# Performance work log

Hardware: AMD Instinct MI355X
Metric: run time of the kernel (lower is better)

## Reference

```python
import jax, jax.numpy as jnp
import numpy as np

N_ATOMS = 200000
N_EDGES = 6400000
N_TYPES = 4
COULOMB = 14.399645478425668  # e^2 / (4 pi eps0) in eV*Angstrom
P_EXP = 0.23
A0 = 0.4685


def _phi(r, c, da):
    # r: (E,), c: (4,), da: (4, E) -> (E,)
    return jnp.sum(c[:, None] * jnp.exp(-r * da), axis=0)


def _dphi(r, c, da):
    return jnp.sum(-c[:, None] * da * jnp.exp(-r * da), axis=0)


def _d2phi(r, c, da):
    return jnp.sum(c[:, None] * da ** 2 * jnp.exp(-r * da), axis=0)


def setup_inputs() -> dict:
    key = jax.random.key(0)
    k1, k2, k3, k4 = jax.random.split(key, 4)
    rij = jax.random.uniform(k1, (N_EDGES,), dtype=jnp.float32) * 2.0 + 0.1
    first_atom = jax.random.randint(k2, (N_EDGES,), 0, N_ATOMS, dtype=jnp.int32)
    second_atom = jax.random.randint(k3, (N_EDGES,), 0, N_ATOMS, dtype=jnp.int32)
    atom_type_index = jax.random.randint(k4, (N_ATOMS,), 0, N_TYPES, dtype=jnp.int32)
    # ASE covalent radii for H, C, N, O (Angstrom) and atomic numbers
    covalent_radii = jnp.array([0.31, 0.76, 0.71, 0.66], dtype=jnp.float32)
    atomic_numbers = jnp.array([1.0, 6.0, 7.0, 8.0], dtype=jnp.float32)
    return {
        "rij": rij,
        "covalent_radii": covalent_radii,
        "atomic_numbers": atomic_numbers,
        "first_atom": first_atom,
        "second_atom": second_atom,
        "atom_type_index": atom_type_index,
        "n_atoms": N_ATOMS,
    }


def reference(rij, covalent_radii, atomic_numbers, first_atom, second_atom, atom_type_index, n_atoms):
    # ZBL 4-term exponential screening coefficients
    c = jnp.array([0.02817, 0.28022, 0.50986, 0.18175], dtype=rij.dtype)
    d = jnp.array([0.20162, 0.4029, 0.94229, 3.1998], dtype=rij.dtype)

    ti = atom_type_index[first_atom]   # (E,)
    tj = atom_type_index[second_atom]  # (E,)
    zi = atomic_numbers[ti]
    zj = atomic_numbers[tj]
    rc = covalent_radii[ti] + covalent_radii[tj]  # outer cutoff per pair

    a = A0 / (zi ** P_EXP + zj ** P_EXP)  # (E,)
    da = d[:, None] / a                    # (4, E)
    factor = COULOMB * zi * zj             # (E,)

    # energy at rij
    e = factor / rij * _phi(rij, c, da)

    # switching polynomial matched at rc (r1 = 0)
    phi_c = _phi(rc, c, da)
    dphi_c = _dphi(rc, c, da)
    d2phi_c = _d2phi(rc, c, da)
    ec = factor / rc * phi_c
    dec = factor / rc * (-phi_c / rc + dphi_c)
    d2ec = factor / rc * (d2phi_c - 2.0 / rc * dphi_c + 2.0 * phi_c / rc ** 2)

    A = (-3.0 * dec + rc * d2ec) / rc ** 2
    B = (2.0 * dec - rc * d2ec) / rc ** 3
    C = -ec + rc * dec / 2.0 - rc * rc * d2ec / 12.0

    e = e + A / 3.0 * rij ** 3 + B / 4.0 * rij ** 4 + C
    e = e / 2.0
    e = jnp.where(rij > rc, jnp.zeros_like(e), e)

    # scatter pair energies onto first atom of each pair
    e_nodes = jax.ops.segment_sum(e, first_atom, num_segments=n_atoms)
    return e_nodes
```

## Files before the change

kernel.cpp:

```cpp
#include <hip/hip_runtime.h>

#define TPB_PACK  256
#define P1_BLOCKS 512
#define P1_TPB    512
#define SB_BITS   14
#define SBS       (1 << SB_BITS)
#define NS_MAX    16
#define P2_TPB    1024
#define R_SUB     24
#define TPB_RED   256
#define CAP_MAX   1024

__global__ __launch_bounds__(TPB_PACK) void zbl_pack(
    const int* __restrict__ types, unsigned int* __restrict__ packed,
    float* __restrict__ fallback, int natoms, int nwords)
{
    int tid = blockIdx.x * TPB_PACK + threadIdx.x;
    int nth = gridDim.x * TPB_PACK;
    for (int w = tid; w < nwords; w += nth) {
        int base = w << 4;
        unsigned int word = 0;
        #pragma unroll
        for (int j = 0; j < 16; ++j) {
            int i = base + j;
            unsigned int t = (i < natoms) ? (unsigned int)types[i] : 0u;
            word |= (t & 3u) << (2 * j);
        }
        packed[w] = word;
    }
    for (int i = tid; i < natoms; i += nth) fallback[i] = 0.0f;
}

__global__ __launch_bounds__(P1_TPB) void zbl_bin(
    const float* __restrict__ rij,
    const float* __restrict__ rcov,
    const float* __restrict__ znum,
    const int*  __restrict__ fa,
    const int*  __restrict__ sa,
    const unsigned int* __restrict__ packed,
    int2*  __restrict__ regions,
    int*   __restrict__ counts,
    float* __restrict__ fallback,
    int E, int nquad, int natoms, int nwords, int NS, int cap, int chunkQ)
{
    extern __shared__ unsigned int s_packed[];
    __shared__ float tab[9][16];
    __shared__ int scnt[NS_MAX];

    for (int w = threadIdx.x; w < nwords; w += P1_TPB)
        s_packed[w] = packed[w];
    if (threadIdx.x < NS) scnt[threadIdx.x] = 0;

    if (threadIdx.x < 16) {
        const float cc[4] = {0.02817f, 0.28022f, 0.50986f, 0.18175f};
        const float dd[4] = {0.20162f, 0.4029f, 0.94229f, 3.1998f};
        const float COUL = 14.399645478425668f;
        int t = threadIdx.x;
        int ti = t >> 2, tj = t & 3;
        float zi = znum[ti], zj = znum[tj];
        float rc = rcov[ti] + rcov[tj];
        float a = 0.4685f / (powf(zi, 0.23f) + powf(zj, 0.23f));
        float inva = 1.0f / a;
        float factor = COUL * zi * zj;
        float da[4], ee[4];
        float phi = 0.0f, dphi = 0.0f, d2phi = 0.0f;
        #pragma unroll
        for (int k = 0; k < 4; ++k) {
            da[k] = dd[k] * inva;
            ee[k] = expf(-rc * da[k]);
            phi   += cc[k] * ee[k];
            dphi  -= cc[k] * da[k] * ee[k];
            d2phi += cc[k] * da[k] * da[k] * ee[k];
        }
        float invrc = 1.0f / rc;
        float ec   = factor * invrc * phi;
        float dec  = factor * invrc * (-phi * invrc + dphi);
        float d2ec = factor * invrc * (d2phi - 2.0f * invrc * dphi + 2.0f * phi * invrc * invrc);
        float A = (-3.0f * dec + rc * d2ec) * invrc * invrc;
        float B = (2.0f * dec - rc * d2ec) * invrc * invrc * invrc;
        float Cc = -ec + 0.5f * rc * dec - rc * rc * d2ec * (1.0f / 12.0f);
        const float L2E = 1.4426950408889634f;
        tab[0][t] = 0.5f * factor;
        tab[1][t] = rc;
        tab[2][t] = -da[0] * L2E;
        tab[3][t] = -da[1] * L2E;
        tab[4][t] = -da[2] * L2E;
        tab[5][t] = -da[3] * L2E;
        tab[6][t] = A * (1.0f / 6.0f);
        tab[7][t] = B * 0.125f;
        tab[8][t] = Cc * 0.5f;
    }
    __syncthreads();

    const float lc0 = -5.1497481f;
    const float lc1 = -1.8353434f;
    const float lc2 = -0.9718340f;
    const float lc3 = -2.4600449f;

    const float4* rij4 = (const float4*)rij;
    const int4*   fa4  = (const int4*)fa;
    const int4*   sa4  = (const int4*)sa;

    size_t myreg = (size_t)blockIdx.x * NS;

    int q0 = blockIdx.x * chunkQ;
    int q1 = q0 + chunkQ; if (q1 > nquad) q1 = nquad;

    for (int q = q0 + threadIdx.x; q < q1; q += P1_TPB) {
        float4 rv = rij4[q];
        int4   iv = fa4[q];
        int4   jv = sa4[q];
        float ra[4] = {rv.x, rv.y, rv.z, rv.w};
        int   ia[4] = {iv.x, iv.y, iv.z, iv.w};
        int   ja[4] = {jv.x, jv.y, jv.z, jv.w};
        int   ta[4];
        #pragma unroll
        for (int k = 0; k < 4; ++k) {
            int i = ia[k], j = ja[k];
            unsigned int wi = s_packed[i >> 4], wj = s_packed[j >> 4];
            unsigned int ti = (wi >> ((i & 15) * 2)) & 3u;
            unsigned int tj = (wj >> ((j & 15) * 2)) & 3u;
            ta[k] = (int)((ti << 2) | tj);
        }
        #pragma unroll
        for (int k = 0; k < 4; ++k) {
            int t = ta[k];
            float r = ra[k];
            if (r <= tab[1][t]) {
                float p = __builtin_amdgcn_exp2f(__builtin_fmaf(r, tab[2][t], lc0))
                        + __builtin_amdgcn_exp2f(__builtin_fmaf(r, tab[3][t], lc1))
                        + __builtin_amdgcn_exp2f(__builtin_fmaf(r, tab[4][t], lc2))
                        + __builtin_amdgcn_exp2f(__builtin_fmaf(r, tab[5][t], lc3));
                float r3 = r * r * r;
                float poly = __builtin_fmaf(__builtin_fmaf(tab[7][t], r, tab[6][t]), r3, tab[8][t]);
                float e = __builtin_fmaf(tab[0][t] * p, __builtin_amdgcn_rcpf(r), poly);
                int atom = ia[k];
                int s = atom >> SB_BITS;
                int slot = atomicAdd(&scnt[s], 1);
                if (slot < cap)
                    regions[(myreg + s) * (size_t)cap + slot] =
                        make_int2(__float_as_int(e), atom);
                else
                    unsafeAtomicAdd(&fallback[atom], e);
            }
        }
    }

    if (blockIdx.x == 0) {
        for (int idx = nquad * 4 + threadIdx.x; idx < E; idx += P1_TPB) {
            int i = fa[idx], j = sa[idx];
            unsigned int wi = s_packed[i >> 4], wj = s_packed[j >> 4];
            int t = (int)((((wi >> ((i & 15) * 2)) & 3u) << 2) |
                           ((wj >> ((j & 15) * 2)) & 3u));
            float r = rij[idx];
            if (r <= tab[1][t]) {
                float p = __builtin_amdgcn_exp2f(__builtin_fmaf(r, tab[2][t], lc0))
                        + __builtin_amdgcn_exp2f(__builtin_fmaf(r, tab[3][t], lc1))
                        + __builtin_amdgcn_exp2f(__builtin_fmaf(r, tab[4][t], lc2))
                        + __builtin_amdgcn_exp2f(__builtin_fmaf(r, tab[5][t], lc3));
                float r3 = r * r * r;
                float poly = __builtin_fmaf(__builtin_fmaf(tab[7][t], r, tab[6][t]), r3, tab[8][t]);
                float e = __builtin_fmaf(tab[0][t] * p, __builtin_amdgcn_rcpf(r), poly);
                unsafeAtomicAdd(&fallback[i], e);
            }
        }
    }

    __syncthreads();
    if (cap > 0 && threadIdx.x < NS)
        counts[threadIdx.x * P1_BLOCKS + blockIdx.x] = min(scnt[threadIdx.x], cap);
}

__global__ __launch_bounds__(P2_TPB) void zbl_agg(
    const int2* __restrict__ regions,
    const int*  __restrict__ counts,
    float* __restrict__ partials,
    int NS, int cap)
{
    __shared__ float acc[SBS];
    int s = blockIdx.x;
    int r = blockIdx.y;
    for (int i = threadIdx.x; i < SBS; i += P2_TPB) acc[i] = 0.0f;
    __syncthreads();

    for (int p = r; p < P1_BLOCKS; p += R_SUB) {
        int n = counts[s * P1_BLOCKS + p];
        size_t base = ((size_t)p * NS + s) * (size_t)cap;
        for (int t = threadIdx.x; t < n; t += P2_TPB) {
            int2 rec = regions[base + t];
            atomicAdd(&acc[rec.y & (SBS - 1)], __int_as_float(rec.x));
        }
    }
    __syncthreads();

    float* dst = partials + ((size_t)s * R_SUB + r) * SBS;
    for (int i = threadIdx.x; i < SBS; i += P2_TPB)
        dst[i] = acc[i];
}

__global__ __launch_bounds__(TPB_RED) void zbl_red(
    const float* __restrict__ partials,
    const float* __restrict__ fallback,
    float* __restrict__ out,
    int natoms)
{
    int atom = blockIdx.x * TPB_RED + threadIdx.x;
    if (atom >= natoms) return;
    int s = atom >> SB_BITS, i = atom & (SBS - 1);
    float acc = fallback[atom];
    const float* p = partials + (size_t)s * R_SUB * SBS + i;
    #pragma unroll
    for (int k = 0; k < R_SUB; ++k) acc += p[(size_t)k * SBS];
    out[atom] = acc;
}

extern "C" void kernel_launch(void* const* d_in, const int* in_sizes, int n_in,
                              void* d_out, int out_size, void* d_ws, size_t ws_size,
                              hipStream_t stream) {
    const float* rij  = (const float*)d_in[0];
    const float* rcov = (const float*)d_in[1];
    const float* znum = (const float*)d_in[2];
    const int*   fa   = (const int*)d_in[3];
    const int*   sa   = (const int*)d_in[4];
    const int*   types= (const int*)d_in[5];
    float* out = (float*)d_out;
    int E = in_sizes[0];
    int natoms = out_size;
    int nquad = E / 4;
    int nwords = (natoms + 15) / 16;
    int NS = (natoms + SBS - 1) >> SB_BITS;
    if (NS > NS_MAX) NS = NS_MAX;
    int chunkQ = (nquad + P1_BLOCKS - 1) / P1_BLOCKS;

    size_t packed_bytes = ((size_t)nwords * 4 + 255) & ~(size_t)255;
    size_t cnt_bytes    = ((size_t)NS * P1_BLOCKS * 4 + 255) & ~(size_t)255;
    size_t fb_bytes     = ((size_t)natoms * 4 + 255) & ~(size_t)255;
    size_t part_bytes   = ((size_t)NS * R_SUB * SBS * 4 + 255) & ~(size_t)255;
    unsigned int* packed = (unsigned int*)d_ws;
    int*   counts   = (int*)  ((char*)d_ws + packed_bytes);
    float* fallback = (float*)((char*)d_ws + packed_bytes + cnt_bytes);
    float* partials = (float*)((char*)d_ws + packed_bytes + cnt_bytes + fb_bytes);
    int2*  regions  = (int2*) ((char*)d_ws + packed_bytes + cnt_bytes
                               + fb_bytes + part_bytes);

    long long avail = (long long)ws_size
                    - (long long)(packed_bytes + cnt_bytes + fb_bytes + part_bytes);
    int cap = 0;
    if (avail > 0) cap = (int)(avail / ((long long)P1_BLOCKS * (long long)NS * 8));
    if (cap > CAP_MAX) cap = CAP_MAX;

    size_t smem = (size_t)nwords * sizeof(unsigned int);

    if (cap >= 64) {
        zbl_pack<<<96, TPB_PACK, 0, stream>>>(types, packed, fallback, natoms, nwords);
        zbl_bin<<<P1_BLOCKS, P1_TPB, smem, stream>>>(
            rij, rcov, znum, fa, sa, packed, regions, counts, fallback,
            E, nquad, natoms, nwords, NS, cap, chunkQ);
        dim3 g2(NS, R_SUB);
        zbl_agg<<<g2, P2_TPB, 0, stream>>>(regions, counts, partials, NS, cap);
        zbl_red<<<(natoms + TPB_RED - 1) / TPB_RED, TPB_RED, 0, stream>>>(
            partials, fallback, out, natoms);
    } else {
        zbl_pack<<<96, TPB_PACK, 0, stream>>>(types, packed, out, natoms, nwords);
        zbl_bin<<<P1_BLOCKS, P1_TPB, smem, stream>>>(
            rij, rcov, znum, fa, sa, packed, regions, counts, out,
            E, nquad, natoms, nwords, NS, 0, chunkQ);
    }
}
```

Baseline: 173.9 us.

## Pack ZBL pair constants into float4 LDS tables and split compute from binning

Replaces the 9x16 scalar shared-memory constant table with two float4 tables and one scalar table, so each edge fetches its per-type-pair constants with wide LDS reads instead of nine scalar ones. The per-edge energy is now computed for all four edges of a quad before any shared-memory counter atomics are issued, which separates the math from the binning stores. The binning kernel's block size also goes from 512 to 1024 threads. This costs extra registers for the buffered energies and changes occupancy and the LDS atomic contention pattern.

```diff
diff --git a/kernel.cpp b/kernel.cpp
--- a/kernel.cpp
+++ b/kernel.cpp
@@ -2,7 +2,7 @@
 
 #define TPB_PACK  256
 #define P1_BLOCKS 512
-#define P1_TPB    512
+#define P1_TPB    1024
 #define SB_BITS   14
 #define SBS       (1 << SB_BITS)
 #define NS_MAX    16
@@ -44,7 +44,9 @@
     int E, int nquad, int natoms, int nwords, int NS, int cap, int chunkQ)
 {
     extern __shared__ unsigned int s_packed[];
-    __shared__ float tab[9][16];
+    __shared__ float4 tabB[16];
+    __shared__ float4 tabA[16];
+    __shared__ float  tabC[16];
     __shared__ int scnt[NS_MAX];
 
     for (int w = threadIdx.x; w < nwords; w += P1_TPB)
@@ -80,15 +82,9 @@
         float B = (2.0f * dec - rc * d2ec) * invrc * invrc * invrc;
         float Cc = -ec + 0.5f * rc * dec - rc * rc * d2ec * (1.0f / 12.0f);
         const float L2E = 1.4426950408889634f;
-        tab[0][t] = 0.5f * factor;
-        tab[1][t] = rc;
-        tab[2][t] = -da[0] * L2E;
-        tab[3][t] = -da[1] * L2E;
-        tab[4][t] = -da[2] * L2E;
-        tab[5][t] = -da[3] * L2E;
-        tab[6][t] = A * (1.0f / 6.0f);
-        tab[7][t] = B * 0.125f;
-        tab[8][t] = Cc * 0.5f;
+        tabB[t] = make_float4(rc, 0.5f * factor, A * (1.0f / 6.0f), B * 0.125f);
+        tabA[t] = make_float4(-da[0] * L2E, -da[1] * L2E, -da[2] * L2E, -da[3] * L2E);
+        tabC[t] = Cc * 0.5f;
     }
     __syncthreads();
 
@@ -122,26 +118,40 @@
             unsigned int tj = (wj >> ((j & 15) * 2)) & 3u;
             ta[k] = (int)((ti << 2) | tj);
         }
+        float eo[4];
+        bool  po[4];
         #pragma unroll
         for (int k = 0; k < 4; ++k) {
             int t = ta[k];
             float r = ra[k];
-            if (r <= tab[1][t]) {
-                float p = __builtin_amdgcn_exp2f(__builtin_fmaf(r, tab[2][t], lc0))
-                        + __builtin_amdgcn_exp2f(__builtin_fmaf(r, tab[3][t], lc1))
-                        + __builtin_amdgcn_exp2f(__builtin_fmaf(r, tab[4][t], lc2))
-                        + __builtin_amdgcn_exp2f(__builtin_fmaf(r, tab[5][t], lc3));
+            float4 B = tabB[t];
+            bool pass = (r <= B.x);
+            po[k] = pass;
+            float e = 0.0f;
+            if (pass) {
+                float4 S = tabA[t];
+                float c2 = tabC[t];
+                float p = __builtin_amdgcn_exp2f(__builtin_fmaf(r, S.x, lc0))
+                        + __builtin_amdgcn_exp2f(__builtin_fmaf(r, S.y, lc1))
+                        + __builtin_amdgcn_exp2f(__builtin_fmaf(r, S.z, lc2))
+                        + __builtin_amdgcn_exp2f(__builtin_fmaf(r, S.w, lc3));
                 float r3 = r * r * r;
-                float poly = __builtin_fmaf(__builtin_fmaf(tab[7][t], r, tab[6][t]), r3, tab[8][t]);
-                float e = __builtin_fmaf(tab[0][t] * p, __builtin_amdgcn_rcpf(r), poly);
+                float poly = __builtin_fmaf(__builtin_fmaf(B.w, r, B.z), r3, c2);
+                e = __builtin_fmaf(B.y * p, __builtin_amdgcn_rcpf(r), poly);
+            }
+            eo[k] = e;
+        }
+        #pragma unroll
+        for (int k = 0; k < 4; ++k) {
+            if (po[k]) {
                 int atom = ia[k];
                 int s = atom >> SB_BITS;
                 int slot = atomicAdd(&scnt[s], 1);
                 if (slot < cap)
                     regions[(myreg + s) * (size_t)cap + slot] =
-                        make_int2(__float_as_int(e), atom);
+                        make_int2(__float_as_int(eo[k]), atom);
                 else
-                    unsafeAtomicAdd(&fallback[atom], e);
+                    unsafeAtomicAdd(&fallback[atom], eo[k]);
             }
         }
     }
@@ -153,14 +163,17 @@
             int t = (int)((((wi >> ((i & 15) * 2)) & 3u) << 2) |
                            ((wj >> ((j & 15) * 2)) & 3u));
             float r = rij[idx];
-            if (r <= tab[1][t]) {
-                float p = __builtin_amdgcn_exp2f(__builtin_fmaf(r, tab[2][t], lc0))
-                        + __builtin_amdgcn_exp2f(__builtin_fmaf(r, tab[3][t], lc1))
-                        + __builtin_amdgcn_exp2f(__builtin_fmaf(r, tab[4][t], lc2))
-                        + __builtin_amdgcn_exp2f(__builtin_fmaf(r, tab[5][t], lc3));
+            float4 B = tabB[t];
+            if (r <= B.x) {
+                float4 S = tabA[t];
+                float c2 = tabC[t];
+                float p = __builtin_amdgcn_exp2f(__builtin_fmaf(r, S.x, lc0))
+                        + __builtin_amdgcn_exp2f(__builtin_fmaf(r, S.y, lc1))
+                        + __builtin_amdgcn_exp2f(__builtin_fmaf(r, S.z, lc2))
+                        + __builtin_amdgcn_exp2f(__builtin_fmaf(r, S.w, lc3));
                 float r3 = r * r * r;
-                float poly = __builtin_fmaf(__builtin_fmaf(tab[7][t], r, tab[6][t]), r3, tab[8][t]);
-                float e = __builtin_fmaf(tab[0][t] * p, __builtin_amdgcn_rcpf(r), poly);
+                float poly = __builtin_fmaf(__builtin_fmaf(B.w, r, B.z), r3, c2);
+                float e = __builtin_fmaf(B.y * p, __builtin_amdgcn_rcpf(r), poly);
                 unsafeAtomicAdd(&fallback[i], e);
             }
         }
```

Result: no change. 172.5 us (-0.8%).
